# Kernel optimization log

Measured on AMD Instinct MI355X. Metric: run time of the kernel, lower is better.

## Reference

```python
import jax, jax.numpy as jnp
import numpy as np

EPS = 1e-6

def _conv(x, w, padding):
    # x: [B,C,H,W], w: [O,I,kh,kw]
    return jax.lax.conv_general_dilated(x, w, window_strides=(1, 1), padding=padding,
                                        dimension_numbers=('NCHW', 'OIHW', 'NCHW'))

def setup_inputs() -> dict:
    key = jax.random.key(0)
    ks = jax.random.split(key, 8)
    C = 512
    B, H, W = 4, 64, 64
    s1 = 1.0 / np.sqrt(C)          # 1x1 conv fan-in
    s3 = 1.0 / np.sqrt(C * 9)      # 3x3 conv fan-in
    return {
        'x': jax.random.normal(ks[0], (B, C, H, W), dtype=jnp.float32),
        'ln_w': jnp.ones((C,), dtype=jnp.float32),
        'ln_b': jnp.zeros((C,), dtype=jnp.float32),
        'wq': jax.random.normal(ks[1], (C, C, 1, 1), dtype=jnp.float32) * s1,
        'wk': jax.random.normal(ks[2], (C, C, 3, 3), dtype=jnp.float32) * s3,
        'wv': jax.random.normal(ks[3], (C, C, 3, 3), dtype=jnp.float32) * s3,
        'wp': jax.random.normal(ks[4], (C, C, 1, 1), dtype=jnp.float32) * s1,
        'bp': jnp.zeros((C,), dtype=jnp.float32),
    }

def reference(x, ln_w, ln_b, wq, wk, wv, wp, bp):
    # channels_first LayerNorm over C
    u = jnp.mean(x, axis=1, keepdims=True)
    s = jnp.mean((x - u) ** 2, axis=1, keepdims=True)
    h = (x - u) / jnp.sqrt(s + EPS)
    h = ln_w[None, :, None, None] * h + ln_b[None, :, None, None]

    q = _conv(h, wq, 'VALID')           # 1x1
    k = _conv(h, wk, [(1, 1), (1, 1)])  # 3x3, pad 1
    v = _conv(h, wv, [(1, 1), (1, 1)])

    b, c, H, W = q.shape
    hw = H * W
    q = q.reshape(b, c, hw)
    k = k.reshape(b, c, hw)
    v = v.reshape(b, c, hw)

    scale = jnp.asarray(int(c) ** (-0.5), q.dtype)
    attn = jnp.einsum('bcm,bcn->bmn', q, k) * scale  # [b, hw_q, hw_k]
    attn = jax.nn.softmax(attn, axis=2)
    out = jnp.einsum('bcn,bmn->bcm', v, attn)        # [b, c, hw_q]
    out = out.reshape(b, c, H, W)

    out = _conv(out, wp, 'VALID') + bp[None, :, None, None]
    return x + out
```

## Files before the change

### kernel.cpp

```cpp
#include <hip/hip_runtime.h>
#include <hip/hip_bf16.h>

#define C_DIM 512
#define HW    4096
#define BATCH 4
#define PW    66
#define PPIX  (PW*PW)

typedef __attribute__((ext_vector_type(8))) short bf16x8;
typedef __attribute__((ext_vector_type(4))) float f32x4;
typedef __attribute__((ext_vector_type(16))) float f32x16;

static __device__ __forceinline__ short f2b(float f) {
    union { float f; unsigned u; } v; v.f = f;
    unsigned r = v.u + 0x7fffu + ((v.u >> 16) & 1u);
    return (short)(r >> 16);
}
static __device__ __forceinline__ float b2f(short s) {
    union { unsigned u; float f; } v; v.u = ((unsigned)(unsigned short)s) << 16;
    return v.f;
}

static __device__ __forceinline__ f32x4 zero4() {
    f32x4 v = {0.f, 0.f, 0.f, 0.f};
    return v;
}
static __device__ __forceinline__ f32x16 zero16() {
    f32x16 v = {0.f,0.f,0.f,0.f, 0.f,0.f,0.f,0.f, 0.f,0.f,0.f,0.f, 0.f,0.f,0.f,0.f};
    return v;
}

static __device__ __forceinline__ void gload16(const void* g, void* l) {
    __builtin_amdgcn_global_load_lds(
        (__attribute__((address_space(1))) void*)g,
        (__attribute__((address_space(3))) void*)l, 16, 0, 0);
}

__global__ void k_cvt_bf16(const float* __restrict__ in, short* __restrict__ out, int n) {
    int i = blockIdx.x * 256 + threadIdx.x;
    if (i < n) out[i] = f2b(in[i]);
}

__global__ void k_reorder_w3(const float* __restrict__ w, short* __restrict__ out) {
    int i = blockIdx.x * 256 + threadIdx.x;
    int c   = i & 511;
    int tap = (i >> 9) % 9;
    int o   = i / (9 * 512);
    out[i] = f2b(w[((size_t)o * 512 + c) * 9 + tap]);
}

__global__ void k_ln_stats(const float* __restrict__ x, float* __restrict__ mean,
                           float* __restrict__ rstd) {
    __shared__ float ss[8][32];
    __shared__ float sq2[8][32];
    int bid = blockIdx.x;
    int t = threadIdx.x;
    int px = t & 31, cg = t >> 5;
    int p = bid * 32 + px;
    int b = p >> 12, pix = p & 4095;
    const float* xp = x + (size_t)b * C_DIM * HW + pix;
    float s = 0.f, sq = 0.f;
    #pragma unroll 4
    for (int c = cg * 64; c < cg * 64 + 64; ++c) {
        float v = xp[(size_t)c * HW];
        s += v; sq += v * v;
    }
    ss[cg][px] = s;
    sq2[cg][px] = sq;
    __syncthreads();
    if (t < 32) {
        float S = 0.f, Q = 0.f;
        #pragma unroll
        for (int j = 0; j < 8; ++j) { S += ss[j][t]; Q += sq2[j][t]; }
        float mu  = S * (1.0f / C_DIM);
        float var = Q * (1.0f / C_DIM) - mu * mu;
        int pg = bid * 32 + t;
        mean[pg] = mu;
        rstd[pg] = 1.0f / sqrtf(var + 1e-6f);
    }
}

__global__ void k_ln_apply(const float* __restrict__ x, const float* __restrict__ mean,
                           const float* __restrict__ rstd, const float* __restrict__ lnw,
                           const float* __restrict__ lnb, short* __restrict__ hp) {
    __shared__ short tile[64][65];
    int bid = blockIdx.x;
    int ct = bid & 7, y = (bid >> 3) & 63, b = bid >> 9;
    int c0 = ct * 64, p0 = y * 64;
    int t = threadIdx.x;
    int pi = t & 63, ci0 = t >> 6;
    int pg = (b << 12) + p0 + pi;
    float mu = mean[pg], rs = rstd[pg];
    const float* xb = x + (size_t)b * C_DIM * HW;
    #pragma unroll
    for (int cc = 0; cc < 64; cc += 4) {
        int c = c0 + cc + ci0;
        float v = xb[(size_t)c * HW + p0 + pi];
        tile[cc + ci0][pi] = f2b((v - mu) * rs * lnw[c] + lnb[c]);
    }
    __syncthreads();
    int cj = t & 63, pj = t >> 6;
    #pragma unroll
    for (int pp = 0; pp < 64; pp += 4) {
        int pidx = pp + pj;
        size_t dst = ((size_t)b * PPIX + (size_t)(y + 1) * PW + 1 + pidx) * C_DIM + c0 + cj;
        hp[dst] = tile[cj][pidx];
    }
}

template<int TAPS, int GMODE, int EPI>
__global__ __launch_bounds__(256, 2) void k_gemm(
        const short* __restrict__ A, const short* __restrict__ Bw,
        void* __restrict__ Out, const float* __restrict__ bias,
        const float* __restrict__ resid)
{
    constexpr int K = TAPS * 512;
    constexpr int NKC = K / 64;
    __shared__ short Alds[128 * 64];
    __shared__ short Blds[128 * 64];
    int bid = blockIdx.x;
    int mt = bid & 31, nt = (bid >> 5) & 3, b = bid >> 7;
    int m0 = mt * 128, n0 = nt * 128;
    int t = threadIdx.x;
    int lane = t & 63, w = t >> 6;
    int wm = w >> 1, wn = w & 1;
    int g = lane >> 4, li = lane & 15;
    int srow = t >> 3, schunk = t & 7;
    const short* Ab = A + (GMODE == 0 ? (size_t)b * PPIX * C_DIM : (size_t)b * HW * C_DIM);

    f32x4 acc[4][4];
    #pragma unroll
    for (int i = 0; i < 4; ++i)
        #pragma unroll
        for (int j = 0; j < 4; ++j) acc[i][j] = zero4();

    for (int kc = 0; kc < NKC; ++kc) {
        int tap = (TAPS == 9) ? (kc >> 3) : 4;
        int cb  = (kc & 7) * 64;
        __syncthreads();
        #pragma unroll
        for (int r = 0; r < 4; ++r) {
            int row = r * 32 + srow;
            size_t goff;
            if (GMODE == 0) {
                int m = m0 + row;
                int yy = m >> 6, xx = m & 63;
                int pp = (yy + tap / 3) * PW + xx + (tap % 3);
                goff = (size_t)pp * C_DIM + cb + schunk * 8;
            } else {
                goff = (size_t)(m0 + row) * K + kc * 64 + schunk * 8;
            }
            gload16(Ab + goff, Alds + row * 64 + schunk * 8);
        }
        #pragma unroll
        for (int r = 0; r < 4; ++r) {
            int row = r * 32 + srow;
            size_t goff = (size_t)(n0 + row) * K + kc * 64 + schunk * 8;
            gload16(Bw + goff, Blds + row * 64 + schunk * 8);
        }
        __syncthreads();
        #pragma unroll
        for (int ks = 0; ks < 2; ++ks) {
            int koff = ks * 32 + g * 8;
            bf16x8 af[4], bfr[4];
            #pragma unroll
            for (int i = 0; i < 4; ++i)
                af[i] = *(const bf16x8*)&Alds[(wm * 64 + i * 16 + li) * 64 + koff];
            #pragma unroll
            for (int j = 0; j < 4; ++j)
                bfr[j] = *(const bf16x8*)&Blds[(wn * 64 + j * 16 + li) * 64 + koff];
            #pragma unroll
            for (int i = 0; i < 4; ++i)
                #pragma unroll
                for (int j = 0; j < 4; ++j)
                    acc[i][j] = __builtin_amdgcn_mfma_f32_16x16x32_bf16(af[i], bfr[j], acc[i][j], 0, 0, 0);
        }
    }
    #pragma unroll
    for (int fm = 0; fm < 4; ++fm) {
        #pragma unroll
        for (int fn = 0; fn < 4; ++fn) {
            int mrow = m0 + wm * 64 + fm * 16 + g * 4;
            int ncol = n0 + wn * 64 + fn * 16 + li;
            if constexpr (EPI == 0) {
                #pragma unroll
                for (int i = 0; i < 4; ++i) {
                    size_t dst = ((size_t)b * HW + mrow + i) * C_DIM + ncol;
                    ((short*)Out)[dst] = f2b(acc[fm][fn][i]);
                }
            } else if constexpr (EPI == 1) {
                size_t dst = ((size_t)b * C_DIM + ncol) * HW + mrow;
                short4 sv = make_short4(f2b(acc[fm][fn][0]), f2b(acc[fm][fn][1]),
                                        f2b(acc[fm][fn][2]), f2b(acc[fm][fn][3]));
                *(short4*)((short*)Out + dst) = sv;
            } else {
                size_t dst = ((size_t)b * C_DIM + ncol) * HW + mrow;
                float bb = bias[ncol];
                float4 xr = *(const float4*)(resid + dst);
                float4 o;
                o.x = acc[fm][fn][0] + bb + xr.x;
                o.y = acc[fm][fn][1] + bb + xr.y;
                o.z = acc[fm][fn][2] + bb + xr.z;
                o.w = acc[fm][fn][3] + bb + xr.w;
                *(float4*)((float*)Out + dst) = o;
            }
        }
    }
}

__global__ __launch_bounds__(256, 2) void k_gemm_kv(
        const short* __restrict__ A, const short* __restrict__ Bk,
        const short* __restrict__ Bv, short* __restrict__ OutK,
        short* __restrict__ OutV)
{
    constexpr int K = 4608;
    __shared__ short Alds[128 * 64];
    __shared__ short Bklds[128 * 64];
    __shared__ short Bvlds[128 * 64];
    int bid = blockIdx.x;
    int mt = bid & 31, nt = (bid >> 5) & 3, b = bid >> 7;
    int m0 = mt * 128, n0 = nt * 128;
    int t = threadIdx.x;
    int lane = t & 63, w = t >> 6;
    int wm = w >> 1, wn = w & 1;
    int g = lane >> 4, li = lane & 15;
    int srow = t >> 3, schunk = t & 7;
    const short* Ab = A + (size_t)b * PPIX * C_DIM;

    f32x4 accK[4][4], accV[4][4];
    #pragma unroll
    for (int i = 0; i < 4; ++i)
        #pragma unroll
        for (int j = 0; j < 4; ++j) { accK[i][j] = zero4(); accV[i][j] = zero4(); }

    for (int kc = 0; kc < 72; ++kc) {
        int tap = kc >> 3;
        int cb  = (kc & 7) * 64;
        __syncthreads();
        #pragma unroll
        for (int r = 0; r < 4; ++r) {
            int row = r * 32 + srow;
            int m = m0 + row;
            int yy = m >> 6, xx = m & 63;
            int pp = (yy + tap / 3) * PW + xx + (tap % 3);
            gload16(Ab + (size_t)pp * C_DIM + cb + schunk * 8, Alds + row * 64 + schunk * 8);
        }
        #pragma unroll
        for (int r = 0; r < 4; ++r) {
            int row = r * 32 + srow;
            size_t goff = (size_t)(n0 + row) * K + kc * 64 + schunk * 8;
            gload16(Bk + goff, Bklds + row * 64 + schunk * 8);
            gload16(Bv + goff, Bvlds + row * 64 + schunk * 8);
        }
        __syncthreads();
        #pragma unroll
        for (int ks = 0; ks < 2; ++ks) {
            int koff = ks * 32 + g * 8;
            bf16x8 af[4], bk[4], bv[4];
            #pragma unroll
            for (int i = 0; i < 4; ++i)
                af[i] = *(const bf16x8*)&Alds[(wm * 64 + i * 16 + li) * 64 + koff];
            #pragma unroll
            for (int j = 0; j < 4; ++j)
                bk[j] = *(const bf16x8*)&Bklds[(wn * 64 + j * 16 + li) * 64 + koff];
            #pragma unroll
            for (int i = 0; i < 4; ++i)
                #pragma unroll
                for (int j = 0; j < 4; ++j)
                    accK[i][j] = __builtin_amdgcn_mfma_f32_16x16x32_bf16(af[i], bk[j], accK[i][j], 0, 0, 0);
            #pragma unroll
            for (int j = 0; j < 4; ++j)
                bv[j] = *(const bf16x8*)&Bvlds[(wn * 64 + j * 16 + li) * 64 + koff];
            #pragma unroll
            for (int i = 0; i < 4; ++i)
                #pragma unroll
                for (int j = 0; j < 4; ++j)
                    accV[i][j] = __builtin_amdgcn_mfma_f32_16x16x32_bf16(af[i], bv[j], accV[i][j], 0, 0, 0);
        }
    }
    #pragma unroll
    for (int fm = 0; fm < 4; ++fm) {
        #pragma unroll
        for (int fn = 0; fn < 4; ++fn) {
            int mrow = m0 + wm * 64 + fm * 16 + g * 4;
            int ncol = n0 + wn * 64 + fn * 16 + li;
            #pragma unroll
            for (int i = 0; i < 4; ++i) {
                size_t dst = ((size_t)b * HW + mrow + i) * C_DIM + ncol;
                OutK[dst] = f2b(accK[fm][fn][i]);
            }
            size_t dstv = ((size_t)b * C_DIM + ncol) * HW + mrow;
            short4 sv = make_short4(f2b(accV[fm][fn][0]), f2b(accV[fm][fn][1]),
                                    f2b(accV[fm][fn][2]), f2b(accV[fm][fn][3]));
            *(short4*)(OutV + dstv) = sv;
        }
    }
}

#define KT 32
#define NTILES 64
__global__ __launch_bounds__(512, 2) void k_attn(
        const short* __restrict__ qT, const short* __restrict__ kT,
        const short* __restrict__ vg, short* __restrict__ O0,
        short* __restrict__ O1, float* __restrict__ L0, float* __restrict__ L1)
{
    __shared__ __align__(16) short pool[78848];
    short* Kp = pool;
    short* Vp = pool + 32768;
    short* Pp = pool + 73728;

    int bid0 = blockIdx.x;
    int bid = (bid0 & 7) * 32 + (bid0 >> 3);
    int qt = bid & 31, ks = (bid >> 5) & 1, b = bid >> 6;
    int m0 = qt * 128;
    int t = threadIdx.x, lane = t & 63, w = t >> 6;
    int g = lane >> 4, li = lane & 15;
    int l31 = lane & 31, l5 = lane >> 5;

    const short* kb = kT + (size_t)b * HW * C_DIM + (size_t)ks * 2048 * C_DIM;
    const short* vb = vg + (size_t)b * C_DIM * HW + ks * 2048;

    bf16x8 qf[16];
    {
        const short* qrow = qT + ((size_t)b * HW + m0 + w * 16 + li) * C_DIM;
        #pragma unroll
        for (int kc = 0; kc < 16; ++kc)
            qf[kc] = *(const bf16x8*)&qrow[kc * 32 + g * 8];
    }
    f32x16 oacc[8];
    #pragma unroll
    for (int a = 0; a < 8; ++a) oacc[a] = zero16();
    float lsum = 0.f;

    const short* ksrc = kb + (size_t)(t & 31) * 512 + (t >> 5) * 8;
    int voff[5];
    #pragma unroll
    for (int r = 0; r < 5; ++r) {
        int D = r * 512 + t;
        int ch = D / 5;
        int c  = D - ch * 5;
        voff[r] = (c < 4) ? ch * 4096 + c * 8 : 0;
    }

    const float SC = 0.044194173824159216f * 1.4426950408889634f;

    auto STAGE = [&](int buf, int nt) {
        int n0 = nt * KT;
        const short* kS = ksrc + (size_t)n0 * 512;
        short* kD = Kp + buf * 16384 + t * 8;
        #pragma unroll
        for (int r = 0; r < 4; ++r)
            gload16(kS + r * 128, kD + r * 4096);
        short* vD = Vp + buf * 20480 + t * 8;
        #pragma unroll
        for (int r = 0; r < 5; ++r)
            gload16(vb + voff[r] + n0, vD + r * 4096);
    };

    STAGE(0, 0);
    asm volatile("s_waitcnt vmcnt(0)" ::: "memory");
    __builtin_amdgcn_s_barrier();
    __builtin_amdgcn_sched_barrier(0);

    int buf = 0;
    for (int nt = 0; nt < NTILES; ++nt) {
        if (nt + 1 < NTILES) STAGE(buf ^ 1, nt + 1);

        const short* kbase = Kp + buf * 16384 + g * 256 + li * 8;
        f32x4 s0[2], s1[2];
        s0[0] = zero4(); s0[1] = zero4(); s1[0] = zero4(); s1[1] = zero4();
        __builtin_amdgcn_s_setprio(1);
        #pragma unroll
        for (int kc = 0; kc < 16; kc += 2) {
            #pragma unroll
            for (int fn = 0; fn < 2; ++fn) {
                bf16x8 ka  = *(const bf16x8*)&kbase[kc * 1024 + fn * 128];
                bf16x8 ka2 = *(const bf16x8*)&kbase[(kc + 1) * 1024 + fn * 128];
                s0[fn] = __builtin_amdgcn_mfma_f32_16x16x32_bf16(ka,  qf[kc],     s0[fn], 0, 0, 0);
                s1[fn] = __builtin_amdgcn_mfma_f32_16x16x32_bf16(ka2, qf[kc + 1], s1[fn], 0, 0, 0);
            }
        }
        __builtin_amdgcn_s_setprio(0);
        #pragma unroll
        for (int fn = 0; fn < 2; ++fn) {
            float e0 = exp2f((s0[fn][0] + s1[fn][0]) * SC);
            float e1 = exp2f((s0[fn][1] + s1[fn][1]) * SC);
            float e2 = exp2f((s0[fn][2] + s1[fn][2]) * SC);
            float e3 = exp2f((s0[fn][3] + s1[fn][3]) * SC);
            lsum += (e0 + e1) + (e2 + e3);
            union { __hip_bfloat162 h; unsigned u; } p01, p23;
            p01.h = __float22bfloat162_rn(make_float2(e0, e1));
            p23.h = __float22bfloat162_rn(make_float2(e2, e3));
            *(uint2*)&Pp[(w * 16 + li) * 40 + fn * 16 + g * 4] = make_uint2(p01.u, p23.u);
        }

        asm volatile("s_waitcnt lgkmcnt(0)" ::: "memory");
        __builtin_amdgcn_s_barrier();
        __builtin_amdgcn_sched_barrier(0);

        const short* vbase = Vp + buf * 20480 + (size_t)w * 64 * 40;
        bf16x8 vf[2][2];
        #pragma unroll
        for (int cht = 0; cht < 2; ++cht)
            #pragma unroll
            for (int kx = 0; kx < 2; ++kx)
                vf[cht][kx] = *(const bf16x8*)&vbase[(cht * 32 + l31) * 40 + kx * 16 + l5 * 8];
        __builtin_amdgcn_s_setprio(1);
        #pragma unroll
        for (int q2 = 0; q2 < 4; ++q2) {
            #pragma unroll
            for (int kx = 0; kx < 2; ++kx) {
                bf16x8 pf = *(const bf16x8*)&Pp[(q2 * 32 + l31) * 40 + kx * 16 + l5 * 8];
                oacc[q2 * 2 + 0] = __builtin_amdgcn_mfma_f32_32x32x16_bf16(vf[0][kx], pf, oacc[q2 * 2 + 0], 0, 0, 0);
                oacc[q2 * 2 + 1] = __builtin_amdgcn_mfma_f32_32x32x16_bf16(vf[1][kx], pf, oacc[q2 * 2 + 1], 0, 0, 0);
            }
        }
        __builtin_amdgcn_s_setprio(0);

        asm volatile("s_waitcnt vmcnt(0)" ::: "memory");
        __builtin_amdgcn_s_barrier();
        __builtin_amdgcn_sched_barrier(0);
        buf ^= 1;
    }

    lsum += __shfl_xor(lsum, 16);
    lsum += __shfl_xor(lsum, 32);
    float* Lb = (ks ? L1 : L0) + (size_t)b * HW + m0 + w * 16;
    if (lane < 16) Lb[lane] = lsum;

    short* tp = pool + w * 9216;
    #pragma unroll
    for (int a = 0; a < 8; ++a) {
        int q2 = a >> 1, cht = a & 1;
        int q_l = q2 * 32 + l31;
        #pragma unroll
        for (int rq = 0; rq < 4; ++rq) {
            int chb = cht * 32 + rq * 8 + l5 * 4;
            union { __hip_bfloat162 h; unsigned u; } x01, x23;
            x01.h = __float22bfloat162_rn(make_float2(oacc[a][rq * 4 + 0], oacc[a][rq * 4 + 1]));
            x23.h = __float22bfloat162_rn(make_float2(oacc[a][rq * 4 + 2], oacc[a][rq * 4 + 3]));
            *(uint2*)&tp[q_l * 72 + chb] = make_uint2(x01.u, x23.u);
        }
    }
    asm volatile("s_waitcnt lgkmcnt(0)" ::: "memory");
    __builtin_amdgcn_sched_barrier(0);
    short* Ob = (ks ? O1 : O0) + ((size_t)b * HW + m0) * C_DIM + w * 64;
    #pragma unroll
    for (int qg = 0; qg < 16; ++qg) {
        int qr = qg * 8 + (lane >> 3);
        bf16x8 v = *(const bf16x8*)&tp[qr * 72 + (lane & 7) * 8];
        *(bf16x8*)&Ob[(size_t)qr * C_DIM + (lane & 7) * 8] = v;
    }
}

__global__ void k_att_comb(const short* __restrict__ O0, const short* __restrict__ O1,
                           const float* __restrict__ L0, const float* __restrict__ L1,
                           short* __restrict__ oatt) {
    int i = blockIdx.x * 256 + threadIdx.x;
    int row = i >> 6;
    int c0 = (i & 63) * 8;
    float r = 1.0f / (L0[row] + L1[row]);
    size_t base = (size_t)row * C_DIM + c0;
    bf16x8 a = *(const bf16x8*)&O0[base];
    bf16x8 c = *(const bf16x8*)&O1[base];
    bf16x8 o;
    #pragma unroll
    for (int j = 0; j < 8; ++j)
        o[j] = f2b((b2f(a[j]) + b2f(c[j])) * r);
    *(bf16x8*)&oatt[base] = o;
}

extern "C" void kernel_launch(void* const* d_in, const int* in_sizes, int n_in,
                              void* d_out, int out_size, void* d_ws, size_t ws_size,
                              hipStream_t stream) {
    const float* x    = (const float*)d_in[0];
    const float* ln_w = (const float*)d_in[1];
    const float* ln_b = (const float*)d_in[2];
    const float* wq   = (const float*)d_in[3];
    const float* wk   = (const float*)d_in[4];
    const float* wv   = (const float*)d_in[5];
    const float* wp   = (const float*)d_in[6];
    const float* bp   = (const float*)d_in[7];
    float* out = (float*)d_out;

    char* ws = (char*)d_ws;
    size_t off = 0;
    auto alloc = [&](size_t bytes) {
        char* p = ws + off;
        off += (bytes + 255) & ~(size_t)255;
        return p;
    };
    short* hp   = (short*)alloc((size_t)BATCH * PPIX * C_DIM * 2);
    short* wqb  = (short*)alloc((size_t)512 * 512 * 2);
    short* wkr  = (short*)alloc((size_t)512 * 4608 * 2);
    short* wvr  = (short*)alloc((size_t)512 * 4608 * 2);
    short* wpb  = (short*)alloc((size_t)512 * 512 * 2);
    short* qT   = (short*)alloc((size_t)BATCH * HW * C_DIM * 2);
    short* kT   = (short*)alloc((size_t)BATCH * HW * C_DIM * 2);
    short* vg   = (short*)alloc((size_t)BATCH * HW * C_DIM * 2);
    short* oatt = (short*)alloc((size_t)BATCH * HW * C_DIM * 2);
    float* mean = (float*)alloc((size_t)BATCH * HW * 4);
    float* rstd = (float*)alloc((size_t)BATCH * HW * 4);

    hipMemsetAsync(hp, 0, (size_t)BATCH * PPIX * C_DIM * 2, stream);
    k_cvt_bf16<<<1024, 256, 0, stream>>>(wq, wqb, 512 * 512);
    k_cvt_bf16<<<1024, 256, 0, stream>>>(wp, wpb, 512 * 512);
    k_reorder_w3<<<9216, 256, 0, stream>>>(wk, wkr);
    k_reorder_w3<<<9216, 256, 0, stream>>>(wv, wvr);
    k_ln_stats<<<512, 256, 0, stream>>>(x, mean, rstd);
    k_ln_apply<<<2048, 256, 0, stream>>>(x, mean, rstd, ln_w, ln_b, hp);

    k_gemm<1, 0, 0><<<512, 256, 0, stream>>>(hp, wqb, qT, nullptr, nullptr);
    k_gemm_kv<<<512, 256, 0, stream>>>(hp, wkr, wvr, kT, vg);

    short* Op0 = hp;
    short* Op1 = oatt;
    float* Ls0 = mean;
    float* Ls1 = rstd;
    k_attn<<<256, 512, 0, stream>>>(qT, kT, vg, Op0, Op1, Ls0, Ls1);
    k_att_comb<<<4096, 256, 0, stream>>>(Op0, Op1, Ls0, Ls1, oatt);

    k_gemm<1, 1, 2><<<512, 256, 0, stream>>>(oatt, wpb, out, bp, x);
}
```

Baseline: 397.3 us.

## Use FP8 MFMA for attention QK^T scores with pre-converted K

Converts K to FP8 in a new pass, reusing the reordered-weight buffer as storage, and converts the Q fragments to FP8 in registers. The QK^T score MFMAs then use the fp8 16x16x32 instruction instead of bf16. This halves K staging traffic and LDS footprint and uses the higher-throughput FP8 matrix path. The cost is an extra conversion kernel and reduced score precision, which may loosen accuracy of the softmax inputs.

New measurement: 376.1 us. 5.3% less time.

```diff
diff --git a/kernel.cpp b/kernel.cpp
--- a/kernel.cpp
+++ b/kernel.cpp
@@ -10,6 +10,7 @@
 typedef __attribute__((ext_vector_type(8))) short bf16x8;
 typedef __attribute__((ext_vector_type(4))) float f32x4;
 typedef __attribute__((ext_vector_type(16))) float f32x16;
+typedef __attribute__((ext_vector_type(2))) long long l64x2;
 
 static __device__ __forceinline__ short f2b(float f) {
     union { float f; unsigned u; } v; v.f = f;
@@ -47,6 +48,20 @@
     int tap = (i >> 9) % 9;
     int o   = i / (9 * 512);
     out[i] = f2b(w[((size_t)o * 512 + c) * 9 + tap]);
+}
+
+__global__ void k_cvt_k8(const short* __restrict__ in, unsigned char* __restrict__ out) {
+    int i = blockIdx.x * 256 + threadIdx.x;
+    int m = i >> 6;
+    int p = (i & 63) * 8;
+    int kcp = p >> 6, g = (p >> 4) & 3, half = (p >> 3) & 1;
+    int chb = (kcp * 2 + half) * 32 + g * 8;
+    bf16x8 v = *(const bf16x8*)&in[(size_t)m * 512 + chb];
+    int lo = __builtin_amdgcn_cvt_pk_fp8_f32(b2f(v[0]), b2f(v[1]), 0, false);
+    lo     = __builtin_amdgcn_cvt_pk_fp8_f32(b2f(v[2]), b2f(v[3]), lo, true);
+    int hi = __builtin_amdgcn_cvt_pk_fp8_f32(b2f(v[4]), b2f(v[5]), 0, false);
+    hi     = __builtin_amdgcn_cvt_pk_fp8_f32(b2f(v[6]), b2f(v[7]), hi, true);
+    *(uint2*)&out[(size_t)m * 512 + p] = make_uint2((unsigned)lo, (unsigned)hi);
 }
 
 __global__ void k_ln_stats(const float* __restrict__ x, float* __restrict__ mean,
@@ -300,14 +315,14 @@
 #define KT 32
 #define NTILES 64
 __global__ __launch_bounds__(512, 2) void k_attn(
-        const short* __restrict__ qT, const short* __restrict__ kT,
+        const short* __restrict__ qT, const unsigned char* __restrict__ kT8,
         const short* __restrict__ vg, short* __restrict__ O0,
         short* __restrict__ O1, float* __restrict__ L0, float* __restrict__ L1)
 {
-    __shared__ __align__(16) short pool[78848];
-    short* Kp = pool;
-    short* Vp = pool + 32768;
-    short* Pp = pool + 73728;
+    __shared__ __align__(16) short pool[73728];
+    unsigned char* Kp8 = (unsigned char*)pool;
+    short* Vp = pool + 16384;
+    short* Pp = pool + 57344;
 
     int bid0 = blockIdx.x;
     int bid = (bid0 & 7) * 32 + (bid0 >> 3);
@@ -317,22 +332,28 @@
     int g = lane >> 4, li = lane & 15;
     int l31 = lane & 31, l5 = lane >> 5;
 
-    const short* kb = kT + (size_t)b * HW * C_DIM + (size_t)ks * 2048 * C_DIM;
+    const unsigned char* kb8 = kT8 + ((size_t)b * HW + (size_t)ks * 2048) * 512;
     const short* vb = vg + (size_t)b * C_DIM * HW + ks * 2048;
 
-    bf16x8 qf[16];
+    long long qf8[16];
     {
         const short* qrow = qT + ((size_t)b * HW + m0 + w * 16 + li) * C_DIM;
         #pragma unroll
-        for (int kc = 0; kc < 16; ++kc)
-            qf[kc] = *(const bf16x8*)&qrow[kc * 32 + g * 8];
+        for (int kc = 0; kc < 16; ++kc) {
+            bf16x8 qv = *(const bf16x8*)&qrow[kc * 32 + g * 8];
+            int lo = __builtin_amdgcn_cvt_pk_fp8_f32(b2f(qv[0]), b2f(qv[1]), 0, false);
+            lo     = __builtin_amdgcn_cvt_pk_fp8_f32(b2f(qv[2]), b2f(qv[3]), lo, true);
+            int hi = __builtin_amdgcn_cvt_pk_fp8_f32(b2f(qv[4]), b2f(qv[5]), 0, false);
+            hi     = __builtin_amdgcn_cvt_pk_fp8_f32(b2f(qv[6]), b2f(qv[7]), hi, true);
+            qf8[kc] = ((long long)(unsigned)hi << 32) | (unsigned)lo;
+        }
     }
     f32x16 oacc[8];
     #pragma unroll
     for (int a = 0; a < 8; ++a) oacc[a] = zero16();
     float lsum = 0.f;
 
-    const short* ksrc = kb + (size_t)(t & 31) * 512 + (t >> 5) * 8;
+    const unsigned char* ksrc8 = kb8 + (size_t)(t & 31) * 512 + (t >> 5) * 16;
     int voff[5];
     #pragma unroll
     for (int r = 0; r < 5; ++r) {
@@ -346,11 +367,10 @@
 
     auto STAGE = [&](int buf, int nt) {
         int n0 = nt * KT;
-        const short* kS = ksrc + (size_t)n0 * 512;
-        short* kD = Kp + buf * 16384 + t * 8;
-        #pragma unroll
-        for (int r = 0; r < 4; ++r)
-            gload16(kS + r * 128, kD + r * 4096);
+        const unsigned char* kS = ksrc8 + (size_t)n0 * 512;
+        unsigned char* kD = Kp8 + buf * 16384 + t * 16;
+        gload16(kS, kD);
+        gload16(kS + 256, kD + 8192);
         short* vD = Vp + buf * 20480 + t * 8;
         #pragma unroll
         for (int r = 0; r < 5; ++r)
@@ -366,18 +386,17 @@
     for (int nt = 0; nt < NTILES; ++nt) {
         if (nt + 1 < NTILES) STAGE(buf ^ 1, nt + 1);
 
-        const short* kbase = Kp + buf * 16384 + g * 256 + li * 8;
+        const unsigned char* kbase8 = Kp8 + buf * 16384 + g * 512 + li * 16;
         f32x4 s0[2], s1[2];
         s0[0] = zero4(); s0[1] = zero4(); s1[0] = zero4(); s1[1] = zero4();
         __builtin_amdgcn_s_setprio(1);
         #pragma unroll
-        for (int kc = 0; kc < 16; kc += 2) {
+        for (int kcp = 0; kcp < 8; ++kcp) {
             #pragma unroll
             for (int fn = 0; fn < 2; ++fn) {
-                bf16x8 ka  = *(const bf16x8*)&kbase[kc * 1024 + fn * 128];
-                bf16x8 ka2 = *(const bf16x8*)&kbase[(kc + 1) * 1024 + fn * 128];
-                s0[fn] = __builtin_amdgcn_mfma_f32_16x16x32_bf16(ka,  qf[kc],     s0[fn], 0, 0, 0);
-                s1[fn] = __builtin_amdgcn_mfma_f32_16x16x32_bf16(ka2, qf[kc + 1], s1[fn], 0, 0, 0);
+                l64x2 kv = *(const l64x2*)&kbase8[kcp * 2048 + fn * 256];
+                s0[fn] = __builtin_amdgcn_mfma_f32_16x16x32_fp8_fp8(kv[0], qf8[2 * kcp],     s0[fn], 0, 0, 0);
+                s1[fn] = __builtin_amdgcn_mfma_f32_16x16x32_fp8_fp8(kv[1], qf8[2 * kcp + 1], s1[fn], 0, 0, 0);
             }
         }
         __builtin_amdgcn_s_setprio(0);
@@ -513,11 +532,14 @@
     k_gemm<1, 0, 0><<<512, 256, 0, stream>>>(hp, wqb, qT, nullptr, nullptr);
     k_gemm_kv<<<512, 256, 0, stream>>>(hp, wkr, wvr, kT, vg);
 
+    unsigned char* kT8 = (unsigned char*)wkr;
+    k_cvt_k8<<<4096, 256, 0, stream>>>(kT, kT8);
+
     short* Op0 = hp;
     short* Op1 = oatt;
     float* Ls0 = mean;
     float* Ls1 = rstd;
-    k_attn<<<256, 512, 0, stream>>>(qT, kT, vg, Op0, Op1, Ls0, Ls1);
+    k_attn<<<256, 512, 0, stream>>>(qT, kT8, vg, Op0, Op1, Ls0, Ls1);
     k_att_comb<<<4096, 256, 0, stream>>>(Op0, Op1, Ls0, Ls1, oatt);
 
     k_gemm<1, 1, 2><<<512, 256, 0, stream>>>(oatt, wpb, out, bp, x);
```
